# Kernel tuning notes

Measured on AMD Instinct MI355X. Metric: run time of the kernel, lower is better.

Reference implementation:

```python
import jax, jax.numpy as jnp
import numpy as np

N, E, D_EMB, D_OUT, K = 4096, 131072, 128, 64, 3


def setup_inputs() -> dict:
    key = jax.random.key(0)
    k1, k2, k3, k4 = jax.random.split(key, 4)
    node_features = jax.random.normal(k1, (N, D_EMB), dtype=jnp.float32)
    edge_index = jax.random.randint(k2, (2, E), 0, N, dtype=jnp.int32)
    edge_weights = jax.random.uniform(k3, (E,), dtype=jnp.float32)
    # xavier_uniform-like init for Emb (shape [embdsize, nin])
    limit = float(np.sqrt(6.0 / (D_EMB + D_OUT)))
    Emb = jax.random.uniform(k4, (D_EMB, D_OUT), dtype=jnp.float32, minval=-limit, maxval=limit)
    return {"node_features": node_features, "Emb": Emb,
            "edge_index": edge_index, "edge_weights": edge_weights}


def reference(node_features, Emb, edge_index, edge_weights):
    # embedding: [N, embdsize] @ [embdsize, nin] -> [N, nin]
    x = node_features @ Emb
    n = x.shape[0]
    A = jnp.zeros((n, n), dtype=x.dtype).at[edge_index[0], edge_index[1]].set(edge_weights)
    # matrix_power(A, K) @ x  ==  K repeated A @ x (associativity), avoids forming A^K
    for _ in range(K):
        x = A @ x
    return x
```

## Files before the change

kernel.cpp:

```cpp
#include <hip/hip_runtime.h>
#include <stdint.h>


#define N_NODES 4096
#define D_EMB   128
#define D_OUT   64

#define CAP       128
#define CAP_SHIFT 7

__global__ void embed_scatter_kernel(const float* __restrict__ nf,
                                     const float* __restrict__ emb,
                                     float* __restrict__ x,
                                     const int* __restrict__ ei,
                                     const float* __restrict__ ew, int E,
                                     int* __restrict__ cnt,
                                     int4* __restrict__ slots) {
    if (blockIdx.x < 1024) {
        __shared__ float srow[4][D_EMB];
        int wave = threadIdx.x >> 6;
        int lane = threadIdx.x & 63;
        int row  = blockIdx.x * 4 + wave;
        float2 a = ((const float2*)(nf + (size_t)row * D_EMB))[lane];
        srow[wave][2 * lane]     = a.x;
        srow[wave][2 * lane + 1] = a.y;
        __syncthreads();
        float acc = 0.0f;
#pragma unroll 8
        for (int k = 0; k < D_EMB; ++k)
            acc = fmaf(srow[wave][k], emb[k * D_OUT + lane], acc);
        x[row * D_OUT + lane] = acc;
    } else {
        int e = (blockIdx.x - 1024) * blockDim.x + threadIdx.x;
        if (e >= E) return;
        int src = ei[e];
        int dst = ei[E + e];
        int idx = atomicAdd(&cnt[src], 1);
        if (idx < CAP) {
            int4 s;
            s.x = dst;
            s.y = __float_as_int(ew[e]);
            s.z = e;
            s.w = 0;
            slots[(src << CAP_SHIFT) + idx] = s;
        }
    }
}

__global__ void dedup_spmm_kernel(const int* __restrict__ cnt,
                                  int4* __restrict__ slots,
                                  const float* __restrict__ x,
                                  float* __restrict__ y) {
    __shared__ int   sdst[4][CAP];
    __shared__ int   seid[4][CAP];
    __shared__ float sw[4][CAP];

    int wave = threadIdx.x >> 6;
    int lane = threadIdx.x & 63;
    int row  = blockIdx.x * 4 + wave;
    int c = cnt[row];
    if (c > CAP) c = CAP;
    int4* s = slots + ((long)row << CAP_SHIFT);

#pragma unroll
    for (int half = 0; half < 2; ++half) {
        int i = lane + half * 64;
        if (i < c) {
            int4 si = s[i];
            sdst[wave][i] = si.x;
            sw[wave][i]   = __int_as_float(si.y);
            seid[wave][i] = si.z;
        }
    }
    __syncthreads();

#pragma unroll
    for (int half = 0; half < 2; ++half) {
        int i = lane + half * 64;
        if (i < c) {
            int d = sdst[wave][i], id = seid[wave][i];
            bool loser = false;
            for (int j = 0; j < c; ++j)
                loser |= (sdst[wave][j] == d) & (seid[wave][j] > id);
            if (loser) {
                sw[wave][i] = 0.0f;
                ((int*)&s[i])[1] = 0;
            }
        }
    }
    __syncthreads();

    float acc = 0.0f;
    int i = 0;
    for (; i + 8 <= c; i += 8) {
        float vw[8], vx[8];
#pragma unroll
        for (int k = 0; k < 8; ++k) vw[k] = sw[wave][i + k];
        int vd[8];
#pragma unroll
        for (int k = 0; k < 8; ++k) vd[k] = sdst[wave][i + k];
#pragma unroll
        for (int k = 0; k < 8; ++k) vx[k] = x[vd[k] * D_OUT + lane];
#pragma unroll
        for (int k = 0; k < 8; ++k) acc = fmaf(vw[k], vx[k], acc);
    }
    for (; i < c; ++i)
        acc = fmaf(sw[wave][i], x[sdst[wave][i] * D_OUT + lane], acc);
    y[row * D_OUT + lane] = acc;
}

__global__ void spmm_kernel(const int* __restrict__ cnt,
                            const int4* __restrict__ slots,
                            const float* __restrict__ x,
                            float* __restrict__ y) {
    __shared__ int   sdst[4][CAP];
    __shared__ float sw[4][CAP];

    int wave = threadIdx.x >> 6;
    int lane = threadIdx.x & 63;
    int row  = blockIdx.x * 4 + wave;
    int c = cnt[row];
    if (c > CAP) c = CAP;
    const int4* s = slots + ((long)row << CAP_SHIFT);

#pragma unroll
    for (int half = 0; half < 2; ++half) {
        int i = lane + half * 64;
        if (i < c) {
            int4 si = s[i];
            sdst[wave][i] = si.x;
            sw[wave][i]   = __int_as_float(si.y);
        }
    }
    __syncthreads();

    float acc = 0.0f;
    int i = 0;
    for (; i + 8 <= c; i += 8) {
        float vw[8], vx[8];
#pragma unroll
        for (int k = 0; k < 8; ++k) vw[k] = sw[wave][i + k];
        int vd[8];
#pragma unroll
        for (int k = 0; k < 8; ++k) vd[k] = sdst[wave][i + k];
#pragma unroll
        for (int k = 0; k < 8; ++k) vx[k] = x[vd[k] * D_OUT + lane];
#pragma unroll
        for (int k = 0; k < 8; ++k) acc = fmaf(vw[k], vx[k], acc);
    }
    for (; i < c; ++i)
        acc = fmaf(sw[wave][i], x[sdst[wave][i] * D_OUT + lane], acc);
    y[row * D_OUT + lane] = acc;
}

extern "C" void kernel_launch(void* const* d_in, const int* in_sizes, int n_in,
                              void* d_out, int out_size, void* d_ws, size_t ws_size,
                              hipStream_t stream) {
    const float* nf  = (const float*)d_in[0];
    const float* emb = (const float*)d_in[1];
    const int*   ei  = (const int*)d_in[2];
    const float* ew  = (const float*)d_in[3];
    float* out = (float*)d_out;

    const int E = in_sizes[3];

    char* ws = (char*)d_ws;
    size_t o = 0;
    auto take = [&](size_t bytes) -> void* {
        void* p = ws + o;
        o += (bytes + 255) & ~(size_t)255;
        return p;
    };
    int*  cnt   = (int*)take((size_t)N_NODES * 4);
    int4* slots = (int4*)take((size_t)N_NODES * CAP * 16);
    float* x0   = (float*)take((size_t)N_NODES * D_OUT * 4);
    float* x1   = (float*)take((size_t)N_NODES * D_OUT * 4);

    const int TB = 256;
    const int NB = N_NODES / 4;
    const int SB = (E + TB - 1) / TB;

    hipMemsetAsync(cnt, 0, (size_t)N_NODES * 4, stream);
    embed_scatter_kernel<<<NB + SB, TB, 0, stream>>>(nf, emb, x0,
                                                     ei, ew, E, cnt, slots);
    dedup_spmm_kernel<<<NB, TB, 0, stream>>>(cnt, slots, x0, x1);
    spmm_kernel<<<NB, TB, 0, stream>>>(cnt, slots, x1, x0);
    spmm_kernel<<<NB, TB, 0, stream>>>(cnt, slots, x0, out);
}
```

Baseline: 44.67 us.

## Fuse embed, scatter and three SpMM passes into one cooperative persistent kernel

Replaces the four separate kernel launches with a single cooperatively launched kernel of 512 blocks that loops over rows per wave. The phases are separated by a hierarchical atomic grid barrier (group counters feeding a root counter), and the barrier counters are cleared by the same memset as the degree counts. This removes per-launch gaps and dispatch overhead between phases. In exchange it adds barrier spin costs, halves the parallelism per phase, and relies on every wave staying in lockstep because the intra-block syncs on shared memory were dropped.

```diff
diff --git a/kernel.cpp b/kernel.cpp
--- a/kernel.cpp
+++ b/kernel.cpp
@@ -6,151 +6,193 @@
 #define D_EMB   128
 #define D_OUT   64
 
-#define CAP       128
+#define CAPN      128
 #define CAP_SHIFT 7
 
-__global__ void embed_scatter_kernel(const float* __restrict__ nf,
-                                     const float* __restrict__ emb,
-                                     float* __restrict__ x,
-                                     const int* __restrict__ ei,
-                                     const float* __restrict__ ew, int E,
-                                     int* __restrict__ cnt,
-                                     int4* __restrict__ slots) {
-    if (blockIdx.x < 1024) {
-        __shared__ float srow[4][D_EMB];
-        int wave = threadIdx.x >> 6;
-        int lane = threadIdx.x & 63;
-        int row  = blockIdx.x * 4 + wave;
+#define NBLK   512
+#define NTHR   256
+#define NWAVES (NBLK * (NTHR / 64))
+#define NGRP   (NBLK / 16)
+
+__device__ __forceinline__ void gbar(int* grp, int* root, int epoch) {
+    __syncthreads();
+    if (threadIdx.x == 0) {
+        __threadfence();
+        int a = atomicAdd(&grp[blockIdx.x >> 4], 1);
+        if (((a + 1) & 15) == 0) atomicAdd(root, 1);
+        const int target = NGRP * epoch;
+        while (__hip_atomic_load(root, __ATOMIC_RELAXED,
+                                 __HIP_MEMORY_SCOPE_AGENT) < target)
+            __builtin_amdgcn_s_sleep(2);
+        __threadfence();
+    }
+    __syncthreads();
+}
+
+__global__ __launch_bounds__(NTHR, 2)
+void fused_kernel(const float* __restrict__ nf,
+                  const float* __restrict__ emb,
+                  const int* __restrict__ ei,
+                  const float* __restrict__ ew,
+                  int E,
+                  float* __restrict__ out,
+                  int* __restrict__ cnt,
+                  int* __restrict__ grp,
+                  int* __restrict__ root,
+                  int4* __restrict__ slots,
+                  float* __restrict__ x0,
+                  float* __restrict__ x1) {
+    __shared__ float srow[4][D_EMB];
+    __shared__ int   sdst[4][CAPN];
+    __shared__ int   seid[4][CAPN];
+    __shared__ float sw[4][CAPN];
+
+    const int tid  = blockIdx.x * NTHR + threadIdx.x;
+    const int wave = threadIdx.x >> 6;
+    const int lane = threadIdx.x & 63;
+    const int gw   = blockIdx.x * (NTHR / 64) + wave;
+
+    if (tid < E) {
+        int src = ei[tid];
+        int dst = ei[E + tid];
+        int idx = atomicAdd(&cnt[src], 1);
+        if (idx < CAPN) {
+            int4 s;
+            s.x = dst;
+            s.y = __float_as_int(ew[tid]);
+            s.z = tid;
+            s.w = 0;
+            slots[(src << CAP_SHIFT) + idx] = s;
+        }
+    }
+
+    for (int row = gw; row < N_NODES; row += NWAVES) {
         float2 a = ((const float2*)(nf + (size_t)row * D_EMB))[lane];
         srow[wave][2 * lane]     = a.x;
         srow[wave][2 * lane + 1] = a.y;
-        __syncthreads();
         float acc = 0.0f;
 #pragma unroll 8
         for (int k = 0; k < D_EMB; ++k)
             acc = fmaf(srow[wave][k], emb[k * D_OUT + lane], acc);
-        x[row * D_OUT + lane] = acc;
-    } else {
-        int e = (blockIdx.x - 1024) * blockDim.x + threadIdx.x;
-        if (e >= E) return;
-        int src = ei[e];
-        int dst = ei[E + e];
-        int idx = atomicAdd(&cnt[src], 1);
-        if (idx < CAP) {
-            int4 s;
-            s.x = dst;
-            s.y = __float_as_int(ew[e]);
-            s.z = e;
-            s.w = 0;
-            slots[(src << CAP_SHIFT) + idx] = s;
-        }
-    }
-}
-
-__global__ void dedup_spmm_kernel(const int* __restrict__ cnt,
-                                  int4* __restrict__ slots,
-                                  const float* __restrict__ x,
-                                  float* __restrict__ y) {
-    __shared__ int   sdst[4][CAP];
-    __shared__ int   seid[4][CAP];
-    __shared__ float sw[4][CAP];
-
-    int wave = threadIdx.x >> 6;
-    int lane = threadIdx.x & 63;
-    int row  = blockIdx.x * 4 + wave;
-    int c = cnt[row];
-    if (c > CAP) c = CAP;
-    int4* s = slots + ((long)row << CAP_SHIFT);
-
-#pragma unroll
-    for (int half = 0; half < 2; ++half) {
-        int i = lane + half * 64;
-        if (i < c) {
-            int4 si = s[i];
-            sdst[wave][i] = si.x;
-            sw[wave][i]   = __int_as_float(si.y);
-            seid[wave][i] = si.z;
-        }
-    }
-    __syncthreads();
-
-#pragma unroll
-    for (int half = 0; half < 2; ++half) {
-        int i = lane + half * 64;
-        if (i < c) {
-            int d = sdst[wave][i], id = seid[wave][i];
-            bool loser = false;
-            for (int j = 0; j < c; ++j)
-                loser |= (sdst[wave][j] == d) & (seid[wave][j] > id);
-            if (loser) {
-                sw[wave][i] = 0.0f;
-                ((int*)&s[i])[1] = 0;
-            }
-        }
-    }
-    __syncthreads();
-
-    float acc = 0.0f;
-    int i = 0;
-    for (; i + 8 <= c; i += 8) {
-        float vw[8], vx[8];
-#pragma unroll
-        for (int k = 0; k < 8; ++k) vw[k] = sw[wave][i + k];
-        int vd[8];
-#pragma unroll
-        for (int k = 0; k < 8; ++k) vd[k] = sdst[wave][i + k];
-#pragma unroll
-        for (int k = 0; k < 8; ++k) vx[k] = x[vd[k] * D_OUT + lane];
-#pragma unroll
-        for (int k = 0; k < 8; ++k) acc = fmaf(vw[k], vx[k], acc);
-    }
-    for (; i < c; ++i)
-        acc = fmaf(sw[wave][i], x[sdst[wave][i] * D_OUT + lane], acc);
-    y[row * D_OUT + lane] = acc;
-}
-
-__global__ void spmm_kernel(const int* __restrict__ cnt,
-                            const int4* __restrict__ slots,
-                            const float* __restrict__ x,
-                            float* __restrict__ y) {
-    __shared__ int   sdst[4][CAP];
-    __shared__ float sw[4][CAP];
-
-    int wave = threadIdx.x >> 6;
-    int lane = threadIdx.x & 63;
-    int row  = blockIdx.x * 4 + wave;
-    int c = cnt[row];
-    if (c > CAP) c = CAP;
-    const int4* s = slots + ((long)row << CAP_SHIFT);
-
-#pragma unroll
-    for (int half = 0; half < 2; ++half) {
-        int i = lane + half * 64;
-        if (i < c) {
-            int4 si = s[i];
-            sdst[wave][i] = si.x;
-            sw[wave][i]   = __int_as_float(si.y);
-        }
-    }
-    __syncthreads();
-
-    float acc = 0.0f;
-    int i = 0;
-    for (; i + 8 <= c; i += 8) {
-        float vw[8], vx[8];
-#pragma unroll
-        for (int k = 0; k < 8; ++k) vw[k] = sw[wave][i + k];
-        int vd[8];
-#pragma unroll
-        for (int k = 0; k < 8; ++k) vd[k] = sdst[wave][i + k];
-#pragma unroll
-        for (int k = 0; k < 8; ++k) vx[k] = x[vd[k] * D_OUT + lane];
-#pragma unroll
-        for (int k = 0; k < 8; ++k) acc = fmaf(vw[k], vx[k], acc);
-    }
-    for (; i < c; ++i)
-        acc = fmaf(sw[wave][i], x[sdst[wave][i] * D_OUT + lane], acc);
-    y[row * D_OUT + lane] = acc;
+        x0[row * D_OUT + lane] = acc;
+    }
+
+    gbar(grp, root, 1);
+
+    for (int row = gw; row < N_NODES; row += NWAVES) {
+        int c = cnt[row];
+        if (c > CAPN) c = CAPN;
+        int4* s = slots + ((long)row << CAP_SHIFT);
+#pragma unroll
+        for (int half = 0; half < 2; ++half) {
+            int i = lane + half * 64;
+            if (i < c) {
+                int4 si = s[i];
+                sdst[wave][i] = si.x;
+                sw[wave][i]   = __int_as_float(si.y);
+                seid[wave][i] = si.z;
+            }
+        }
+#pragma unroll
+        for (int half = 0; half < 2; ++half) {
+            int i = lane + half * 64;
+            if (i < c) {
+                int d = sdst[wave][i], id = seid[wave][i];
+                bool loser = false;
+                for (int j = 0; j < c; ++j)
+                    loser |= (sdst[wave][j] == d) & (seid[wave][j] > id);
+                if (loser) {
+                    sw[wave][i] = 0.0f;
+                    ((int*)&s[i])[1] = 0;
+                }
+            }
+        }
+        float acc = 0.0f;
+        int i = 0;
+        for (; i + 8 <= c; i += 8) {
+            float vw[8], vx[8];
+            int vd[8];
+#pragma unroll
+            for (int k = 0; k < 8; ++k) vw[k] = sw[wave][i + k];
+#pragma unroll
+            for (int k = 0; k < 8; ++k) vd[k] = sdst[wave][i + k];
+#pragma unroll
+            for (int k = 0; k < 8; ++k) vx[k] = x0[vd[k] * D_OUT + lane];
+#pragma unroll
+            for (int k = 0; k < 8; ++k) acc = fmaf(vw[k], vx[k], acc);
+        }
+        for (; i < c; ++i)
+            acc = fmaf(sw[wave][i], x0[sdst[wave][i] * D_OUT + lane], acc);
+        x1[row * D_OUT + lane] = acc;
+    }
+
+    gbar(grp, root, 2);
+
+    for (int row = gw; row < N_NODES; row += NWAVES) {
+        int c = cnt[row];
+        if (c > CAPN) c = CAPN;
+        const int4* s = slots + ((long)row << CAP_SHIFT);
+#pragma unroll
+        for (int half = 0; half < 2; ++half) {
+            int i = lane + half * 64;
+            if (i < c) {
+                int4 si = s[i];
+                sdst[wave][i] = si.x;
+                sw[wave][i]   = __int_as_float(si.y);
+            }
+        }
+        float acc = 0.0f;
+        int i = 0;
+        for (; i + 8 <= c; i += 8) {
+            float vw[8], vx[8];
+            int vd[8];
+#pragma unroll
+            for (int k = 0; k < 8; ++k) vw[k] = sw[wave][i + k];
+#pragma unroll
+            for (int k = 0; k < 8; ++k) vd[k] = sdst[wave][i + k];
+#pragma unroll
+            for (int k = 0; k < 8; ++k) vx[k] = x1[vd[k] * D_OUT + lane];
+#pragma unroll
+            for (int k = 0; k < 8; ++k) acc = fmaf(vw[k], vx[k], acc);
+        }
+        for (; i < c; ++i)
+            acc = fmaf(sw[wave][i], x1[sdst[wave][i] * D_OUT + lane], acc);
+        x0[row * D_OUT + lane] = acc;
+    }
+
+    gbar(grp, root, 3);
+
+    for (int row = gw; row < N_NODES; row += NWAVES) {
+        int c = cnt[row];
+        if (c > CAPN) c = CAPN;
+        const int4* s = slots + ((long)row << CAP_SHIFT);
+#pragma unroll
+        for (int half = 0; half < 2; ++half) {
+            int i = lane + half * 64;
+            if (i < c) {
+                int4 si = s[i];
+                sdst[wave][i] = si.x;
+                sw[wave][i]   = __int_as_float(si.y);
+            }
+        }
+        float acc = 0.0f;
+        int i = 0;
+        for (; i + 8 <= c; i += 8) {
+            float vw[8], vx[8];
+            int vd[8];
+#pragma unroll
+            for (int k = 0; k < 8; ++k) vw[k] = sw[wave][i + k];
+#pragma unroll
+            for (int k = 0; k < 8; ++k) vd[k] = sdst[wave][i + k];
+#pragma unroll
+            for (int k = 0; k < 8; ++k) vx[k] = x0[vd[k] * D_OUT + lane];
+#pragma unroll
+            for (int k = 0; k < 8; ++k) acc = fmaf(vw[k], vx[k], acc);
+        }
+        for (; i < c; ++i)
+            acc = fmaf(sw[wave][i], x0[sdst[wave][i] * D_OUT + lane], acc);
+        out[row * D_OUT + lane] = acc;
+    }
 }
 
 extern "C" void kernel_launch(void* const* d_in, const int* in_sizes, int n_in,
@@ -162,7 +204,7 @@
     const float* ew  = (const float*)d_in[3];
     float* out = (float*)d_out;
 
-    const int E = in_sizes[3];
+    int E = in_sizes[3];
 
     char* ws = (char*)d_ws;
     size_t o = 0;
@@ -171,19 +213,19 @@
         o += (bytes + 255) & ~(size_t)255;
         return p;
     };
-    int*  cnt   = (int*)take((size_t)N_NODES * 4);
-    int4* slots = (int4*)take((size_t)N_NODES * CAP * 16);
+    int*  cnt  = (int*)take((size_t)N_NODES * 4);
+    int*  grp  = (int*)take((size_t)NGRP * 4 + 4);
+    int*  root = grp + NGRP;
+    size_t zero_bytes = o;
+    int4* slots = (int4*)take((size_t)N_NODES * CAPN * 16);
     float* x0   = (float*)take((size_t)N_NODES * D_OUT * 4);
     float* x1   = (float*)take((size_t)N_NODES * D_OUT * 4);
 
-    const int TB = 256;
-    const int NB = N_NODES / 4;
-    const int SB = (E + TB - 1) / TB;
-
-    hipMemsetAsync(cnt, 0, (size_t)N_NODES * 4, stream);
-    embed_scatter_kernel<<<NB + SB, TB, 0, stream>>>(nf, emb, x0,
-                                                     ei, ew, E, cnt, slots);
-    dedup_spmm_kernel<<<NB, TB, 0, stream>>>(cnt, slots, x0, x1);
-    spmm_kernel<<<NB, TB, 0, stream>>>(cnt, slots, x1, x0);
-    spmm_kernel<<<NB, TB, 0, stream>>>(cnt, slots, x0, out);
+    hipMemsetAsync(cnt, 0, zero_bytes, stream);
+
+    void* args[] = {(void*)&nf, (void*)&emb, (void*)&ei, (void*)&ew, (void*)&E,
+                    (void*)&out, (void*)&cnt, (void*)&grp, (void*)&root,
+                    (void*)&slots, (void*)&x0, (void*)&x1};
+    hipLaunchCooperativeKernel((const void*)fused_kernel, dim3(NBLK), dim3(NTHR),
+                               args, 0, stream);
 }
```

New measurement: 140.5 us. +214.6%, slower.
